# Optimization experiments

Measured on AMD Instinct MI355X. Metric: run time of the kernel, lower is better.

## Reference

```python
import jax, jax.numpy as jnp
import numpy as np

D = 512  # token_dim == hidden_dim
K = 65536  # number of trajectory tokens


def safe_normalize(v, eps=1e-6):
    n = jnp.linalg.norm(v, axis=-1, keepdims=True)
    ok = n > eps
    e1 = jnp.zeros_like(v).at[..., 0].set(1.0)
    return jnp.where(ok, v / jnp.maximum(n, eps), e1)


def rot6d_to_matrix(x, eps=1e-6):
    # x: (K, 6) -> R: (K, 3, 3), rows (a1, b2, a3)
    a1 = safe_normalize(x[..., 0:3], eps)
    a2 = x[..., 3:6]
    proj = jnp.sum(a1 * a2, axis=-1, keepdims=True) * a1
    b2 = safe_normalize(a2 - proj, eps)
    a3 = safe_normalize(jnp.cross(a1, b2), eps)
    b2 = safe_normalize(jnp.cross(a3, a1), eps)
    return jnp.stack((a1, b2, a3), axis=-2)


def geodesic_angle(R_pred, R_gt, eps=1e-8):
    # RtR = R_gt^T @ R_pred, per-element (K,3,3)
    RtR = jnp.einsum('kji,kjl->kil', R_gt, R_pred)
    trace = RtR[..., 0, 0] + RtR[..., 1, 1] + RtR[..., 2, 2]
    c = jnp.clip((trace - 1.0) * 0.5, -1.0 + 1e-6, 1.0 - 1e-6)
    skew = RtR - jnp.swapaxes(RtR, -1, -2)
    v = jnp.stack([skew[..., 2, 1], skew[..., 0, 2], skew[..., 1, 0]], axis=-1)
    s = 0.5 * jnp.linalg.norm(v, axis=-1) + eps
    return jnp.arctan2(s, c)


def huber(pred, target, beta, mask):
    # smooth-L1 with beta, masked mean (denominator = clamped mask sum)
    d = jnp.abs(pred - target)
    l = jnp.where(d < beta, 0.5 * d * d / beta, d - 0.5 * beta) * mask
    return l.sum() / jnp.maximum(mask.sum(), 1.0)


def rot_loss_fn(pred, gt):
    # pred, gt: (K, 12) = [L rot6d(6), R rot6d(6)]
    Lp, Rp = pred[:, :6], pred[:, 6:]
    Lt, Rt = gt[:, :6], gt[:, 6:]
    Lvalid = jnp.all(Lt != -1000.0, axis=-1)
    Rvalid = jnp.all(Rt != -1000.0, axis=-1)
    safe6 = jnp.array([1.0, 0.0, 0.0, 0.0, 1.0, 0.0], pred.dtype)
    Lt = jnp.where(Lvalid[:, None], Lt, safe6)
    Rt = jnp.where(Rvalid[:, None], Rt, safe6)
    ang_L = geodesic_angle(rot6d_to_matrix(Lp), rot6d_to_matrix(Lt))
    ang_R = geodesic_angle(rot6d_to_matrix(Rp), rot6d_to_matrix(Rt))
    wL = Lvalid.astype(pred.dtype)
    wR = Rvalid.astype(pred.dtype)
    denom = jnp.maximum(wL.sum() + wR.sum(), 1e-8)
    num = jnp.sum(wL * jnp.where(Lvalid, ang_L, 0.0)) + jnp.sum(wR * jnp.where(Rvalid, ang_R, 0.0))
    return num / denom


def _heads(hidden_states, w1, b1, w2, b2, w3, b3):
    # 4 stacked MLPs (m = time, coord, coord2d, quat), torch Linear layout (out, in)
    h1 = jax.nn.relu(jnp.einsum('kc,mhc->mkh', hidden_states, w1) + b1[:, None, :])
    h2 = jax.nn.relu(jnp.einsum('mkh,mgh->mkg', h1, w2) + b2[:, None, :])
    pred_time = h2[0] @ w3[0:1].T + b3[0:1]      # (K, 1)
    pred_coords = h2[1] @ w3[1:7].T + b3[1:7]    # (K, 6)
    pred_2d = h2[2] @ w3[7:11].T + b3[7:11]      # (K, 4)
    pred_quat = h2[3] @ w3[11:23].T + b3[11:23]  # (K, 12)
    return pred_time, pred_coords, pred_2d, pred_quat


def _loss(pred_time, pred_coords, pred_2d, pred_quat, gt,
          beta_3d=0.07, beta_2d=0.02, beta_time=3.0, sigma_time=3.0):
    time_gt = gt[:, 0:1]
    time_valid = (time_gt != -1000.0).astype(jnp.float32)
    xyz_gt = gt[:, 1:7]
    xyz_valid = (xyz_gt != -1000.0).astype(jnp.float32)
    uv_gt = gt[:, 7:11]
    uv_valid = (uv_gt != -1000.0).astype(jnp.float32)
    quat_gt = gt[:, 11:23]
    quat_valid = (quat_gt != -1000.0).astype(jnp.float32)

    time_loss = huber(pred_time, time_gt, beta_time, time_valid)

    dt = jnp.abs(pred_time - time_gt)
    w_t = jnp.where(time_valid.sum() > 0,
                    jnp.exp(-0.5 * (dt / sigma_time) ** 2) * time_valid,
                    jnp.ones_like(pred_time))  # (K, 1), broadcasts over feature dims

    loss_3d = huber(pred_coords, xyz_gt, beta_3d, xyz_valid * w_t)
    loss_2d = huber(pred_2d / 1408.0, uv_gt / 1408.0, beta_2d, uv_valid * w_t)
    quat_huber = huber(pred_quat, quat_gt, 0.2, quat_valid * w_t)
    rot_l = 0.15 * rot_loss_fn(pred_quat, quat_gt)

    return 1.0 * time_loss + 2.0 * loss_3d + 0.5 * loss_2d + 0.5 * quat_huber + rot_l


def setup_inputs() -> dict:
    key = jax.random.key(0)
    ks = jax.random.split(key, 6)
    s = 1.0 / np.sqrt(D)
    return {
        'hidden_states': jax.random.normal(ks[0], (K, D), jnp.float32),
        'gt_traj': jax.random.uniform(ks[1], (K, 23), jnp.float32),
        'w1': jax.random.normal(ks[2], (4, D, D), jnp.float32) * s,
        'b1': jnp.zeros((4, D), jnp.float32),
        'w2': jax.random.normal(ks[3], (4, D, D), jnp.float32) * s,
        'b2': jnp.zeros((4, D), jnp.float32),
        'w3': jax.random.normal(ks[4], (23, D), jnp.float32) * s,
        'b3': jnp.zeros((23,), jnp.float32),
    }


def reference(hidden_states, gt_traj, w1, b1, w2, b2, w3, b3):
    pred_time, pred_coords, pred_2d, pred_quat = _heads(hidden_states, w1, b1, w2, b2, w3, b3)
    total_loss = _loss(pred_time, pred_coords, pred_2d, pred_quat, gt_traj)
    packed = jnp.concatenate(
        [pred_coords.reshape(-1, 2, 3), pred_quat.reshape(-1, 2, 6)], axis=-1
    ).reshape(-1, 18)
    return pred_time, packed, total_loss
```

## Files before the change

kernel.cpp:

```cpp
#include <hip/hip_runtime.h>
#include <math.h>


#define KROWS 65536
#define DH 512

typedef _Float16 f16;
typedef _Float16 half8 __attribute__((ext_vector_type(8)));
typedef float floatx4 __attribute__((ext_vector_type(4)));

#define WS_WF16   0
#define WS_W3F16  4194304
#define WS_PRED2D 4227072
#define WS_PART   5275648

__device__ __forceinline__ void glds16(const void* g, void* l) {
  __builtin_amdgcn_global_load_lds(
      (const __attribute__((address_space(1))) void*)g,
      (__attribute__((address_space(3))) void*)l, 16, 0, 0);
}

__global__ __launch_bounds__(256) void convert_weights(
    const float* __restrict__ w1, const float* __restrict__ w2,
    const float* __restrict__ w3, f16* __restrict__ wf16, f16* __restrict__ w3f16)
{
  int t = blockIdx.x * 256 + threadIdx.x;
  if (t < 262144) {
    int ml = t >> 15;
    int mm = ml >> 1, l = ml & 1;
    int r = t & 32767;
    int fb = r >> 6;
    int lane = r & 63;
    int nt = fb >> 4, kq = fb & 15;
    int n = nt * 16 + (lane & 15);
    int k = kq * 32 + (lane >> 4) * 8;
    const float* src = (l ? w2 : w1) + (size_t)mm * 262144 + n * 512 + k;
    floatx4 u0 = *(const floatx4*)(src);
    floatx4 u1 = *(const floatx4*)(src + 4);
    half8 h;
    h[0] = (f16)u0[0]; h[1] = (f16)u0[1]; h[2] = (f16)u0[2]; h[3] = (f16)u0[3];
    h[4] = (f16)u1[0]; h[5] = (f16)u1[1]; h[6] = (f16)u1[2]; h[7] = (f16)u1[3];
    *(half8*)(wf16 + (size_t)ml * 262144 + fb * 512 + lane * 8) = h;
  } else {
    int j = t - 262144;
    if (j < 23 * DH) w3f16[j] = (f16)w3[j];
  }
}

extern __shared__ unsigned char smem[];

__global__ __launch_bounds__(512, 4) void fused_kernel(
    const float* __restrict__ hidden,
    const f16* __restrict__ wf16,
    const f16* __restrict__ w3f16,
    const float* __restrict__ b1g,
    const float* __restrict__ b2g,
    const float* __restrict__ b3g,
    float* __restrict__ dout,
    float* __restrict__ pred2d)
{
  const int bid = blockIdx.x;
  const int rr  = bid & 7;
  const int m   = rr >> 1;
  const int row_tile = ((bid >> 3) << 1) | (rr & 1);
  const int r0  = row_tile * 64;
  const int tid = threadIdx.x;
  const int w   = __builtin_amdgcn_readfirstlane(tid >> 6);
  const int lane = tid & 63;
  const int l15 = lane & 15;
  const int lg  = lane >> 4;

  unsigned char* h1b = smem;
  unsigned char* astg = smem + 65536;

  const int ra0 = l15 * 128 + (((lg * 2)     ^ (l15 & 7)) << 4);
  const int ra1 = l15 * 128 + (((lg * 2 + 1) ^ (l15 & 7)) << 4);
  const int arow = l15 * 128;
  const int ao   = (lg * 16) ^ ((l15 & 7) << 4);
  const f16* bptr = wf16 + (size_t)(m * 2) * 262144 + lane * 8;
  const int gsrow = 8 * w + (lane >> 3);
  const float* aglp = hidden + (size_t)(r0 + gsrow) * DH
                    + (((lane & 7) ^ ((lane >> 3) & 7)) << 2);
  unsigned char* gldst = astg + w * 1024;

  auto astage = [&](int kc) {
    glds16(aglp + kc * 32, gldst + (kc & 1) * 8192);
  };
  auto areadf32 = [&](const unsigned char* chunk, int mt) -> half8 {
    floatx4 u0 = *(const floatx4*)(chunk + mt * 2048 + ra0);
    floatx4 u1 = *(const floatx4*)(chunk + mt * 2048 + ra1);
    half8 a;
    a[0] = (f16)u0[0]; a[1] = (f16)u0[1]; a[2] = (f16)u0[2]; a[3] = (f16)u0[3];
    a[4] = (f16)u1[0]; a[5] = (f16)u1[1]; a[6] = (f16)u1[2]; a[7] = (f16)u1[3];
    return a;
  };
  auto aread = [&](const unsigned char* chunk, int mt, int kq) -> half8 {
    return *(const half8*)(chunk + mt * 2048 + arow + (ao ^ (kq << 6)));
  };
  auto bload = [&](int l, int g, int nt) -> half8 {
    return *(const half8*)(bptr + l * 262144 + ((w * 4 + nt) * 16 + g) * 512);
  };

  floatx4 acc[4][4];
  const floatx4 zf = {0.f, 0.f, 0.f, 0.f};

  astage(0);
#pragma unroll
  for (int mt = 0; mt < 4; ++mt)
#pragma unroll
    for (int nt = 0; nt < 4; ++nt) acc[mt][nt] = zf;
  __syncthreads();

#pragma unroll 1
  for (int kc = 0; kc < 16; ++kc) {
    if (kc < 15) astage(kc + 1);
    half8 b0 = bload(0, kc, 0), b1 = bload(0, kc, 1),
          b2 = bload(0, kc, 2), b3 = bload(0, kc, 3);
    const unsigned char* chunk = astg + (kc & 1) * 8192;
#pragma unroll
    for (int mt = 0; mt < 4; ++mt) {
      half8 a = areadf32(chunk, mt);
      acc[mt][0] = __builtin_amdgcn_mfma_f32_16x16x32_f16(a, b0, acc[mt][0], 0, 0, 0);
      acc[mt][1] = __builtin_amdgcn_mfma_f32_16x16x32_f16(a, b1, acc[mt][1], 0, 0, 0);
      acc[mt][2] = __builtin_amdgcn_mfma_f32_16x16x32_f16(a, b2, acc[mt][2], 0, 0, 0);
      acc[mt][3] = __builtin_amdgcn_mfma_f32_16x16x32_f16(a, b3, acc[mt][3], 0, 0, 0);
    }
    __syncthreads();
  }

  {
    unsigned char* myc = h1b + w * 8192;
#pragma unroll
    for (int nt = 0; nt < 4; ++nt) {
      const float bv = b1g[m * DH + w * 64 + nt * 16 + l15];
      const int cb = 2 * (nt * 16 + l15);
#pragma unroll
      for (int mt = 0; mt < 4; ++mt)
#pragma unroll
        for (int j = 0; j < 4; ++j) {
          float v = fmaxf(acc[mt][nt][j] + bv, 0.f);
          int row = mt * 16 + 4 * lg + j;
          *(f16*)(myc + row * 128 + (cb ^ ((row & 7) << 4))) = (f16)v;
        }
    }
  }
  __syncthreads();

#pragma unroll
  for (int mt = 0; mt < 4; ++mt)
#pragma unroll
    for (int nt = 0; nt < 4; ++nt) acc[mt][nt] = zf;

#pragma unroll 1
  for (int kc = 0; kc < 8; ++kc) {
    const unsigned char* chunk = h1b + kc * 8192;
#pragma unroll
    for (int gi = 0; gi < 2; ++gi) {
      const int g = kc * 2 + gi;
      half8 b0 = bload(1, g, 0), b1 = bload(1, g, 1),
            b2 = bload(1, g, 2), b3 = bload(1, g, 3);
#pragma unroll
      for (int mt = 0; mt < 4; ++mt) {
        half8 a = aread(chunk, mt, gi);
        acc[mt][0] = __builtin_amdgcn_mfma_f32_16x16x32_f16(a, b0, acc[mt][0], 0, 0, 0);
        acc[mt][1] = __builtin_amdgcn_mfma_f32_16x16x32_f16(a, b1, acc[mt][1], 0, 0, 0);
        acc[mt][2] = __builtin_amdgcn_mfma_f32_16x16x32_f16(a, b2, acc[mt][2], 0, 0, 0);
        acc[mt][3] = __builtin_amdgcn_mfma_f32_16x16x32_f16(a, b3, acc[mt][3], 0, 0, 0);
      }
    }
  }
  __syncthreads();

  {
    unsigned char* myc = h1b + w * 8192;
#pragma unroll
    for (int nt = 0; nt < 4; ++nt) {
      const float bv = b2g[m * DH + w * 64 + nt * 16 + l15];
      const int cb = 2 * (nt * 16 + l15);
#pragma unroll
      for (int mt = 0; mt < 4; ++mt)
#pragma unroll
        for (int j = 0; j < 4; ++j) {
          float v = fmaxf(acc[mt][nt][j] + bv, 0.f);
          int row = mt * 16 + 4 * lg + j;
          *(f16*)(myc + row * 128 + (cb ^ ((row & 7) << 4))) = (f16)v;
        }
    }
  }
  __syncthreads();

  if (w < 4) {
    const int base_m = (m == 0) ? 0 : (m == 1) ? 1 : (m == 2) ? 7 : 11;
    const int cnt_m  = (m == 0) ? 1 : (m == 1) ? 6 : (m == 2) ? 4 : 12;
    const bool ovalid = l15 < cnt_m;
    const f16* w3row = w3f16 + (size_t)(base_m + (ovalid ? l15 : 0)) * DH;
    const half8 hz = {(f16)0, (f16)0, (f16)0, (f16)0, (f16)0, (f16)0, (f16)0, (f16)0};
    floatx4 acc3 = zf;
#pragma unroll
    for (int q = 0; q < 16; ++q) {
      half8 ah = aread(h1b + (q >> 1) * 8192, w, q & 1);
      half8 wv = ovalid ? *(const half8*)(w3row + q * 32 + lg * 8) : hz;
      acc3 = __builtin_amdgcn_mfma_f32_16x16x32_f16(ah, wv, acc3, 0, 0, 0);
    }
    if (ovalid) {
      const float bo = b3g[base_m + l15];
#pragma unroll
      for (int j = 0; j < 4; ++j) {
        const int row = r0 + w * 16 + 4 * lg + j;
        const float v = acc3[j] + bo;
        if (m == 0)      { if (l15 == 0) dout[row] = v; }
        else if (m == 1) { dout[KROWS + row * 18 + (l15 < 3 ? l15 : l15 + 6)] = v; }
        else if (m == 2) { pred2d[row * 4 + l15] = v; }
        else             { dout[KROWS + row * 18 + (l15 < 6 ? l15 + 3 : l15 + 6)] = v; }
      }
    }
  }
}

__device__ __forceinline__ void safe_norm3(float x, float y, float z, float* o) {
  float n = sqrtf(x * x + y * y + z * z);
  if (n > 1e-6f) { o[0] = x / n; o[1] = y / n; o[2] = z / n; }
  else           { o[0] = 1.f;   o[1] = 0.f;   o[2] = 0.f; }
}

__device__ __forceinline__ void rot6d(const float* x, float* R) {
  float a1[3]; safe_norm3(x[0], x[1], x[2], a1);
  float d = a1[0] * x[3] + a1[1] * x[4] + a1[2] * x[5];
  float b2[3]; safe_norm3(x[3] - d * a1[0], x[4] - d * a1[1], x[5] - d * a1[2], b2);
  float a3[3];
  safe_norm3(a1[1] * b2[2] - a1[2] * b2[1],
             a1[2] * b2[0] - a1[0] * b2[2],
             a1[0] * b2[1] - a1[1] * b2[0], a3);
  float bb[3];
  safe_norm3(a3[1] * a1[2] - a3[2] * a1[1],
             a3[2] * a1[0] - a3[0] * a1[2],
             a3[0] * a1[1] - a3[1] * a1[0], bb);
  R[0] = a1[0]; R[1] = a1[1]; R[2] = a1[2];
  R[3] = bb[0]; R[4] = bb[1]; R[5] = bb[2];
  R[6] = a3[0]; R[7] = a3[1]; R[8] = a3[2];
}

__device__ __forceinline__ float geo_angle(const float* P, const float* G) {
  float M[9];
#pragma unroll
  for (int i = 0; i < 3; ++i)
#pragma unroll
    for (int l = 0; l < 3; ++l)
      M[i * 3 + l] = G[0 + i] * P[0 + l] + G[3 + i] * P[3 + l] + G[6 + i] * P[6 + l];
  float tr = M[0] + M[4] + M[8];
  float c = fminf(fmaxf((tr - 1.f) * 0.5f, -1.f + 1e-6f), 1.f - 1e-6f);
  float v0 = M[7] - M[5], v1 = M[2] - M[6], v2 = M[3] - M[1];
  float s = 0.5f * sqrtf(v0 * v0 + v1 * v1 + v2 * v2) + 1e-8f;
  return atan2f(s, c);
}

__global__ __launch_bounds__(256) void loss_partial(
    const float* __restrict__ gt, const float* __restrict__ dout,
    const float* __restrict__ pred2d, float* __restrict__ partials)
{
  const int r = blockIdx.x * 256 + threadIdx.x;
  const float* g  = gt + (size_t)r * 23;
  const float* pk = dout + KROWS + (size_t)r * 18;
  float a[17];

  const float pt = dout[r];
  const float tg = g[0];
  const float tv = (tg != -1000.f) ? 1.f : 0.f;
  const float dt = fabsf(pt - tg);
  a[0] = ((dt < 3.f) ? (0.5f * dt * dt / 3.f) : (dt - 1.5f)) * tv;
  a[1] = tv;
  a[2] = tv;
  const float wt = expf(-0.5f * (dt / 3.f) * (dt / 3.f)) * tv;

  float n3T = 0.f, d3T = 0.f, n3F = 0.f, d3F = 0.f;
#pragma unroll
  for (int j = 0; j < 6; ++j) {
    const float p = pk[j < 3 ? j : j + 6];
    const float q = g[1 + j];
    const float val = (q != -1000.f) ? 1.f : 0.f;
    const float d = fabsf(p - q);
    const float l = (d < 0.07f) ? (0.5f * d * d / 0.07f) : (d - 0.035f);
    n3T += l * val * wt; d3T += val * wt; n3F += l * val; d3F += val;
  }
  a[3] = n3T; a[4] = d3T; a[5] = n3F; a[6] = d3F;

  float n2T = 0.f, d2T = 0.f, n2F = 0.f, d2F = 0.f;
#pragma unroll
  for (int j = 0; j < 4; ++j) {
    const float p = pred2d[(size_t)r * 4 + j];
    const float q = g[7 + j];
    const float val = (q != -1000.f) ? 1.f : 0.f;
    const float d = fabsf(p / 1408.f - q / 1408.f);
    const float l = (d < 0.02f) ? (0.5f * d * d / 0.02f) : (d - 0.01f);
    n2T += l * val * wt; d2T += val * wt; n2F += l * val; d2F += val;
  }
  a[7] = n2T; a[8] = d2T; a[9] = n2F; a[10] = d2F;

  float qp[12];
#pragma unroll
  for (int j = 0; j < 12; ++j) qp[j] = pk[j < 6 ? j + 3 : j + 6];
  float nqT = 0.f, dqT = 0.f, nqF = 0.f, dqF = 0.f;
#pragma unroll
  for (int j = 0; j < 12; ++j) {
    const float q = g[11 + j];
    const float val = (q != -1000.f) ? 1.f : 0.f;
    const float d = fabsf(qp[j] - q);
    const float l = (d < 0.2f) ? (0.5f * d * d / 0.2f) : (d - 0.1f);
    nqT += l * val * wt; dqT += val * wt; nqF += l * val; dqF += val;
  }
  a[11] = nqT; a[12] = dqT; a[13] = nqF; a[14] = dqF;

  bool Lv = true, Rv = true;
#pragma unroll
  for (int j = 0; j < 6; ++j) {
    if (g[11 + j] == -1000.f) Lv = false;
    if (g[17 + j] == -1000.f) Rv = false;
  }
  const float safe6[6] = {1.f, 0.f, 0.f, 0.f, 1.f, 0.f};
  float Lt[6], Rt[6];
#pragma unroll
  for (int j = 0; j < 6; ++j) {
    Lt[j] = Lv ? g[11 + j] : safe6[j];
    Rt[j] = Rv ? g[17 + j] : safe6[j];
  }
  float Rp[9], Rg[9];
  rot6d(qp, Rp);     rot6d(Lt, Rg);
  const float angL = geo_angle(Rp, Rg);
  rot6d(qp + 6, Rp); rot6d(Rt, Rg);
  const float angR = geo_angle(Rp, Rg);
  a[15] = (Lv ? angL : 0.f) + (Rv ? angR : 0.f);
  a[16] = (Lv ? 1.f : 0.f) + (Rv ? 1.f : 0.f);

#pragma unroll
  for (int i = 0; i < 17; ++i) {
    float v = a[i];
#pragma unroll
    for (int off = 32; off > 0; off >>= 1) v += __shfl_down(v, off, 64);
    a[i] = v;
  }
  __shared__ float red[4][17];
  if ((threadIdx.x & 63) == 0) {
    const int wv = threadIdx.x >> 6;
#pragma unroll
    for (int i = 0; i < 17; ++i) red[wv][i] = a[i];
  }
  __syncthreads();
  if (threadIdx.x < 17)
    partials[blockIdx.x * 20 + threadIdx.x] =
        red[0][threadIdx.x] + red[1][threadIdx.x] + red[2][threadIdx.x] + red[3][threadIdx.x];
}

__global__ void loss_final(const float* __restrict__ partials, float* __restrict__ dout)
{
  __shared__ float s[17];
  const int i = threadIdx.x;
  if (i < 17) {
    float v = 0.f;
    for (int b = 0; b < 256; ++b) v += partials[b * 20 + i];
    s[i] = v;
  }
  __syncthreads();
  if (i == 0) {
    const bool flag = s[2] > 0.f;
    const float time_loss = s[0] / fmaxf(s[1], 1.f);
    const float l3 = flag ? s[3] / fmaxf(s[4], 1.f) : s[5] / fmaxf(s[6], 1.f);
    const float l2 = flag ? s[7] / fmaxf(s[8], 1.f) : s[9] / fmaxf(s[10], 1.f);
    const float lq = flag ? s[11] / fmaxf(s[12], 1.f) : s[13] / fmaxf(s[14], 1.f);
    const float rot = 0.15f * (s[15] / fmaxf(s[16], 1e-8f));
    dout[19 * KROWS] = time_loss + 2.f * l3 + 0.5f * l2 + 0.5f * lq + rot;
  }
}

extern "C" void kernel_launch(void* const* d_in, const int* in_sizes, int n_in,
                              void* d_out, int out_size, void* d_ws, size_t ws_size,
                              hipStream_t stream) {
  (void)in_sizes; (void)n_in; (void)out_size; (void)ws_size;
  const float* hidden = (const float*)d_in[0];
  const float* gt     = (const float*)d_in[1];
  const float* w1     = (const float*)d_in[2];
  const float* b1     = (const float*)d_in[3];
  const float* w2     = (const float*)d_in[4];
  const float* b2     = (const float*)d_in[5];
  const float* w3     = (const float*)d_in[6];
  const float* b3     = (const float*)d_in[7];
  float* dout = (float*)d_out;

  unsigned char* ws = (unsigned char*)d_ws;
  f16*   wf16     = (f16*)(ws + WS_WF16);
  f16*   w3f16    = (f16*)(ws + WS_W3F16);
  float* pred2d   = (float*)(ws + WS_PRED2D);
  float* partials = (float*)(ws + WS_PART);

  static bool attr_done = false;
  if (!attr_done) {
    hipFuncSetAttribute(reinterpret_cast<const void*>(fused_kernel),
                        hipFuncAttributeMaxDynamicSharedMemorySize, 81920);
    attr_done = true;
  }

  convert_weights<<<1070, 256, 0, stream>>>(w1, w2, w3, wf16, w3f16);
  fused_kernel<<<4096, 512, 81920, stream>>>(hidden, wf16, w3f16, b1, b2, b3, dout, pred2d);
  loss_partial<<<256, 256, 0, stream>>>(gt, dout, pred2d, partials);
  loss_final<<<1, 64, 0, stream>>>(partials, dout);
}
```

Before: 376.8 us.

## Load hidden-state A operand directly from global, drop LDS staging buffer

```diff
diff --git a/kernel.cpp b/kernel.cpp
--- a/kernel.cpp
+++ b/kernel.cpp
@@ -13,12 +13,6 @@
 #define WS_W3F16  4194304
 #define WS_PRED2D 4227072
 #define WS_PART   5275648
-
-__device__ __forceinline__ void glds16(const void* g, void* l) {
-  __builtin_amdgcn_global_load_lds(
-      (const __attribute__((address_space(1))) void*)g,
-      (__attribute__((address_space(3))) void*)l, 16, 0, 0);
-}
 
 __global__ __launch_bounds__(256) void convert_weights(
     const float* __restrict__ w1, const float* __restrict__ w2,
@@ -70,66 +64,54 @@
   const int l15 = lane & 15;
   const int lg  = lane >> 4;
 
-  unsigned char* h1b = smem;
-  unsigned char* astg = smem + 65536;
-
-  const int ra0 = l15 * 128 + (((lg * 2)     ^ (l15 & 7)) << 4);
-  const int ra1 = l15 * 128 + (((lg * 2 + 1) ^ (l15 & 7)) << 4);
+  unsigned char* hb = smem;
+
   const int arow = l15 * 128;
   const int ao   = (lg * 16) ^ ((l15 & 7) << 4);
-  const f16* bptr = wf16 + (size_t)(m * 2) * 262144 + lane * 8;
-  const int gsrow = 8 * w + (lane >> 3);
-  const float* aglp = hidden + (size_t)(r0 + gsrow) * DH
-                    + (((lane & 7) ^ ((lane >> 3) & 7)) << 2);
-  unsigned char* gldst = astg + w * 1024;
-
-  auto astage = [&](int kc) {
-    glds16(aglp + kc * 32, gldst + (kc & 1) * 8192);
+  auto aread = [&](const unsigned char* base, int g, int mt) -> half8 {
+    return *(const half8*)(base + (g >> 1) * 8192 + mt * 2048 + arow
+                           + (ao ^ ((g & 1) << 6)));
   };
-  auto areadf32 = [&](const unsigned char* chunk, int mt) -> half8 {
-    floatx4 u0 = *(const floatx4*)(chunk + mt * 2048 + ra0);
-    floatx4 u1 = *(const floatx4*)(chunk + mt * 2048 + ra1);
+  const float* aptr = hidden + (size_t)(r0 + l15) * DH + lg * 8;
+  auto aload = [&](int mt, int g) -> half8 {
+    const float* p = aptr + mt * (16 * DH) + g * 32;
+    floatx4 u0 = *(const floatx4*)(p);
+    floatx4 u1 = *(const floatx4*)(p + 4);
     half8 a;
     a[0] = (f16)u0[0]; a[1] = (f16)u0[1]; a[2] = (f16)u0[2]; a[3] = (f16)u0[3];
     a[4] = (f16)u1[0]; a[5] = (f16)u1[1]; a[6] = (f16)u1[2]; a[7] = (f16)u1[3];
     return a;
   };
-  auto aread = [&](const unsigned char* chunk, int mt, int kq) -> half8 {
-    return *(const half8*)(chunk + mt * 2048 + arow + (ao ^ (kq << 6)));
-  };
+  const f16* bptr = wf16 + (size_t)(m * 2) * 262144 + lane * 8;
   auto bload = [&](int l, int g, int nt) -> half8 {
     return *(const half8*)(bptr + l * 262144 + ((w * 4 + nt) * 16 + g) * 512);
   };
 
   floatx4 acc[4][4];
   const floatx4 zf = {0.f, 0.f, 0.f, 0.f};
-
-  astage(0);
+  const half8 hz = {(f16)0, (f16)0, (f16)0, (f16)0, (f16)0, (f16)0, (f16)0, (f16)0};
+
 #pragma unroll
   for (int mt = 0; mt < 4; ++mt)
 #pragma unroll
     for (int nt = 0; nt < 4; ++nt) acc[mt][nt] = zf;
-  __syncthreads();
 
 #pragma unroll 1
-  for (int kc = 0; kc < 16; ++kc) {
-    if (kc < 15) astage(kc + 1);
-    half8 b0 = bload(0, kc, 0), b1 = bload(0, kc, 1),
-          b2 = bload(0, kc, 2), b3 = bload(0, kc, 3);
-    const unsigned char* chunk = astg + (kc & 1) * 8192;
+  for (int g = 0; g < 16; ++g) {
+    half8 c0 = bload(0, g, 0), c1 = bload(0, g, 1),
+          c2 = bload(0, g, 2), c3 = bload(0, g, 3);
 #pragma unroll
     for (int mt = 0; mt < 4; ++mt) {
-      half8 a = areadf32(chunk, mt);
-      acc[mt][0] = __builtin_amdgcn_mfma_f32_16x16x32_f16(a, b0, acc[mt][0], 0, 0, 0);
-      acc[mt][1] = __builtin_amdgcn_mfma_f32_16x16x32_f16(a, b1, acc[mt][1], 0, 0, 0);
-      acc[mt][2] = __builtin_amdgcn_mfma_f32_16x16x32_f16(a, b2, acc[mt][2], 0, 0, 0);
-      acc[mt][3] = __builtin_amdgcn_mfma_f32_16x16x32_f16(a, b3, acc[mt][3], 0, 0, 0);
-    }
-    __syncthreads();
+      half8 a = aload(mt, g);
+      acc[mt][0] = __builtin_amdgcn_mfma_f32_16x16x32_f16(a, c0, acc[mt][0], 0, 0, 0);
+      acc[mt][1] = __builtin_amdgcn_mfma_f32_16x16x32_f16(a, c1, acc[mt][1], 0, 0, 0);
+      acc[mt][2] = __builtin_amdgcn_mfma_f32_16x16x32_f16(a, c2, acc[mt][2], 0, 0, 0);
+      acc[mt][3] = __builtin_amdgcn_mfma_f32_16x16x32_f16(a, c3, acc[mt][3], 0, 0, 0);
+    }
   }
 
   {
-    unsigned char* myc = h1b + w * 8192;
+    unsigned char* myc = hb + w * 8192;
 #pragma unroll
     for (int nt = 0; nt < 4; ++nt) {
       const float bv = b1g[m * DH + w * 64 + nt * 16 + l15];
@@ -152,27 +134,22 @@
     for (int nt = 0; nt < 4; ++nt) acc[mt][nt] = zf;
 
 #pragma unroll 1
-  for (int kc = 0; kc < 8; ++kc) {
-    const unsigned char* chunk = h1b + kc * 8192;
-#pragma unroll
-    for (int gi = 0; gi < 2; ++gi) {
-      const int g = kc * 2 + gi;
-      half8 b0 = bload(1, g, 0), b1 = bload(1, g, 1),
-            b2 = bload(1, g, 2), b3 = bload(1, g, 3);
-#pragma unroll
-      for (int mt = 0; mt < 4; ++mt) {
-        half8 a = aread(chunk, mt, gi);
-        acc[mt][0] = __builtin_amdgcn_mfma_f32_16x16x32_f16(a, b0, acc[mt][0], 0, 0, 0);
-        acc[mt][1] = __builtin_amdgcn_mfma_f32_16x16x32_f16(a, b1, acc[mt][1], 0, 0, 0);
-        acc[mt][2] = __builtin_amdgcn_mfma_f32_16x16x32_f16(a, b2, acc[mt][2], 0, 0, 0);
-        acc[mt][3] = __builtin_amdgcn_mfma_f32_16x16x32_f16(a, b3, acc[mt][3], 0, 0, 0);
-      }
+  for (int g = 0; g < 16; ++g) {
+    half8 c0 = bload(1, g, 0), c1 = bload(1, g, 1),
+          c2 = bload(1, g, 2), c3 = bload(1, g, 3);
+#pragma unroll
+    for (int mt = 0; mt < 4; ++mt) {
+      half8 a = aread(hb, g, mt);
+      acc[mt][0] = __builtin_amdgcn_mfma_f32_16x16x32_f16(a, c0, acc[mt][0], 0, 0, 0);
+      acc[mt][1] = __builtin_amdgcn_mfma_f32_16x16x32_f16(a, c1, acc[mt][1], 0, 0, 0);
+      acc[mt][2] = __builtin_amdgcn_mfma_f32_16x16x32_f16(a, c2, acc[mt][2], 0, 0, 0);
+      acc[mt][3] = __builtin_amdgcn_mfma_f32_16x16x32_f16(a, c3, acc[mt][3], 0, 0, 0);
     }
   }
   __syncthreads();
 
   {
-    unsigned char* myc = h1b + w * 8192;
+    unsigned char* myc = hb + w * 8192;
 #pragma unroll
     for (int nt = 0; nt < 4; ++nt) {
       const float bv = b2g[m * DH + w * 64 + nt * 16 + l15];
@@ -194,11 +171,10 @@
     const int cnt_m  = (m == 0) ? 1 : (m == 1) ? 6 : (m == 2) ? 4 : 12;
     const bool ovalid = l15 < cnt_m;
     const f16* w3row = w3f16 + (size_t)(base_m + (ovalid ? l15 : 0)) * DH;
-    const half8 hz = {(f16)0, (f16)0, (f16)0, (f16)0, (f16)0, (f16)0, (f16)0, (f16)0};
     floatx4 acc3 = zf;
-#pragma unroll
+#pragma unroll 2
     for (int q = 0; q < 16; ++q) {
-      half8 ah = aread(h1b + (q >> 1) * 8192, w, q & 1);
+      half8 ah = aread(hb, q, w);
       half8 wv = ovalid ? *(const half8*)(w3row + q * 32 + lg * 8) : hz;
       acc3 = __builtin_amdgcn_mfma_f32_16x16x32_f16(ah, wv, acc3, 0, 0, 0);
     }
@@ -394,12 +370,12 @@
   static bool attr_done = false;
   if (!attr_done) {
     hipFuncSetAttribute(reinterpret_cast<const void*>(fused_kernel),
-                        hipFuncAttributeMaxDynamicSharedMemorySize, 81920);
+                        hipFuncAttributeMaxDynamicSharedMemorySize, 65536);
     attr_done = true;
   }
 
   convert_weights<<<1070, 256, 0, stream>>>(w1, w2, w3, wf16, w3f16);
-  fused_kernel<<<4096, 512, 81920, stream>>>(hidden, wf16, w3f16, b1, b2, b3, dout, pred2d);
+  fused_kernel<<<4096, 512, 65536, stream>>>(hidden, wf16, w3f16, b1, b2, b3, dout, pred2d);
   loss_partial<<<256, 256, 0, stream>>>(gt, dout, pred2d, partials);
   loss_final<<<1, 64, 0, stream>>>(partials, dout);
 }
```

New measurement: 652.0 us. 73.1% more time.
